# Performance work log

Measured on AMD Instinct MI355X. Metric: run time of the kernel, lower is better.

## Reference

```python
import jax, jax.numpy as jnp
import numpy as np

CODEBOOK_SIZE = 1024
EMB_DIM = 256
BETA = 0.25


def setup_inputs() -> dict:
    key = jax.random.key(0)
    k1, k2 = jax.random.split(key)
    z = jax.random.normal(k1, (8, EMB_DIM, 16, 16, 16), dtype=jnp.float32)
    # torch init: uniform(-1/K, 1/K)
    emb = jax.random.uniform(k2, (CODEBOOK_SIZE, EMB_DIM), dtype=jnp.float32,
                             minval=-1.0 / CODEBOOK_SIZE, maxval=1.0 / CODEBOOK_SIZE)
    return {"z": z, "emb": emb}


def reference(z, emb):
    b, c, h, w, dd = z.shape
    K = emb.shape[0]
    # (b c h w d) -> (b h w d, c)
    zf = jnp.transpose(z, (0, 2, 3, 4, 1)).reshape(-1, c)  # [N, C]
    d = ((zf ** 2).sum(axis=1, keepdims=True)
         + (emb ** 2).sum(axis=1)
         - 2.0 * zf @ emb.T)  # [N, K]
    mean_distance = jnp.mean(d)
    idx = jnp.argmin(d, axis=1)  # [N]
    # one-hot @ codebook == gather
    zq = jnp.take(emb, idx, axis=0)  # [N, C]
    zq = jnp.transpose(zq.reshape(b, h, w, dd, c), (0, 4, 1, 2, 3))  # [b,c,h,w,d]
    loss = (jnp.mean((jax.lax.stop_gradient(zq) - z) ** 2)
            + BETA * jnp.mean((zq - jax.lax.stop_gradient(z)) ** 2))
    # straight-through estimator
    zq_st = z + jax.lax.stop_gradient(zq - z)
    # perplexity from code usage histogram (== mean of one-hot encodings)
    counts = jnp.zeros((K,), dtype=z.dtype).at[idx].add(1.0)
    e_mean = counts / idx.shape[0]
    perplexity = jnp.exp(-jnp.sum(e_mean * jnp.log(e_mean + 1e-10)))
    return zq_st, loss, perplexity, idx, mean_distance
```

## Files before the change

### kernel.cpp

```cpp
#include <hip/hip_runtime.h>
#include <math.h>

#define C 256
#define K 1024
#define SS 4096
#define NB 8
#define NN 32768
#define ZQ_ELEMS 8388608
#define OUT_LOSS 8388608
#define OUT_PERP 8388609
#define OUT_IDX  8388610
#define OUT_MD   8421378

#define WS_SZ2   0
#define WS_SE2   1
#define WS_LOSS  2
#define WS_ZSUM  8
#define WS_ESUM  264
#define WS_CNT   520
#define WS_E2R   1544
#define WS_Z2N   2568
#define WS_FLG   35336
#define WS_EH    68608
#define WS_CAND  330752

#define TC_FACT 1.8e-6f
#define TF_FACT 1.6e-6f
#define CAP 4
#define CAP_BIG 24
#define OV 7

typedef __attribute__((ext_vector_type(8))) short short8;
typedef __attribute__((ext_vector_type(4))) float f32x4;
typedef unsigned short u16;

__device__ inline u16 f2bf(float x) {
  unsigned u = __float_as_uint(x);
  unsigned r = (u + 0x7fffu + ((u >> 16) & 1u)) >> 16;
  return (u16)r;
}
__device__ inline float bf2f(u16 h) { return __uint_as_float(((unsigned)h) << 16); }

__device__ __forceinline__ void gl_lds16(const u16* g, u16* l) {
  __builtin_amdgcn_global_load_lds(
      (const __attribute__((address_space(1))) unsigned int*)g,
      (__attribute__((address_space(3))) unsigned int*)l,
      16, 0, 0);
}

__device__ inline float np_sumsq_256(const float* __restrict__ a) {
  float tot = 0.f;
  #pragma unroll
  for (int h = 0; h < 2; ++h) {
    const float* p = a + 128 * h;
    float r[8];
    #pragma unroll
    for (int j = 0; j < 8; ++j) r[j] = __fmul_rn(p[j], p[j]);
    for (int i = 8; i < 128; i += 8) {
      #pragma unroll
      for (int j = 0; j < 8; ++j) {
        float v = p[i + j];
        r[j] = __fadd_rn(r[j], __fmul_rn(v, v));
      }
    }
    float s01 = __fadd_rn(r[0], r[1]);
    float s23 = __fadd_rn(r[2], r[3]);
    float s45 = __fadd_rn(r[4], r[5]);
    float s67 = __fadd_rn(r[6], r[7]);
    float res = __fadd_rn(__fadd_rn(s01, s23), __fadd_rn(s45, s67));
    tot = (h == 0) ? res : __fadd_rn(tot, res);
  }
  return tot;
}

__global__ __launch_bounds__(256)
void emb_prep_k(const float* __restrict__ emb, float* __restrict__ ws,
                u16* __restrict__ eh) {
  int r0 = blockIdx.x * 16;
  int t = threadIdx.x;
  float s = 0.f;
  #pragma unroll
  for (int i = 0; i < 16; ++i) {
    size_t idx = (size_t)(r0 + i) * C + t;
    float v = emb[idx];
    s += v;
    eh[idx] = f2bf(v);
  }
  atomicAdd(&ws[WS_ESUM + t], s);
  if (t < 16) {
    float e2 = np_sumsq_256(emb + (size_t)(r0 + t) * C);
    ws[WS_E2R + r0 + t] = e2;
    atomicAdd(&ws[WS_SE2], e2);
  }
}

#define MROWS 64
#define ZS_STRIDE 260

__global__ __launch_bounds__(256)
void prep_z_k(const float* __restrict__ z, float* __restrict__ ws,
              u16* __restrict__ zh_g) {
  __shared__ float zs[MROWS * ZS_STRIDE];
  const int t = threadIdx.x;
  const int n0 = blockIdx.x * MROWS;
  const int b = n0 / SS;
  const int s0 = n0 % SS;
  {
    const int sl = t & 63, cg = t >> 6;
    const float* zb = z + (size_t)b * C * SS + s0 + sl;
    #pragma unroll
    for (int i = 0; i < 16; ++i) {
      int c = (cg * 16 + i) * 4;
      float4 v;
      v.x = zb[(size_t)(c + 0) * SS];
      v.y = zb[(size_t)(c + 1) * SS];
      v.z = zb[(size_t)(c + 2) * SS];
      v.w = zb[(size_t)(c + 3) * SS];
      *(float4*)&zs[sl * ZS_STRIDE + c] = v;
    }
  }
  __syncthreads();
  {
    float s = 0.f;
    #pragma unroll 8
    for (int r = 0; r < MROWS; ++r) s += zs[r * ZS_STRIDE + t];
    atomicAdd(&ws[WS_ZSUM + t], s);
  }
  {
    #pragma unroll
    for (int i = 0; i < 8; ++i) {
      int q = i * 256 + t;
      int row = q >> 5;
      int c0 = (q & 31) * 8;
      float4 va = *(const float4*)&zs[row * ZS_STRIDE + c0];
      float4 vb = *(const float4*)&zs[row * ZS_STRIDE + c0 + 4];
      float f[8] = {va.x, va.y, va.z, va.w, vb.x, vb.y, vb.z, vb.w};
      short8 hv;
      #pragma unroll
      for (int j = 0; j < 8; ++j) hv[j] = (short)f2bf(f[j]);
      *(short8*)&zh_g[(size_t)(n0 + row) * C + c0] = hv;
    }
  }
  if (t < MROWS) {
    float z2 = np_sumsq_256(&zs[t * ZS_STRIDE]);
    ws[WS_Z2N + n0 + t] = z2;
    #pragma unroll
    for (int off = 32; off; off >>= 1) z2 += __shfl_down(z2, off);
    if (t == 0) atomicAdd(&ws[WS_SZ2], z2);
  }
}

#define BM 64
#define BN 128
#define CH 64

__global__ __launch_bounds__(256, 2)
void vq_mfma_k(const u16* __restrict__ zh_g, const u16* __restrict__ eh_g,
               const float* __restrict__ e2row, const float* __restrict__ z2np,
               float* __restrict__ out_idx,
               int* __restrict__ qarr, u16* __restrict__ cand) {
  extern __shared__ u16 smem_u16[];
  u16* Bh4 = smem_u16;
  float* e2all = (float*)(Bh4 + 4 * BN * CH);
  float* z2s  = e2all + K;
  float* lval = z2s + BM;
  unsigned* Mlds = (unsigned*)(lval + BM * CAP_BIG);
  unsigned* cntl = Mlds + BM;
  u16* lidx = (u16*)(cntl + BM);

  const int t = threadIdx.x;
  const int lane = t & 63;
  const int wid = t >> 6;
  const int wm = wid >> 1, wn = wid & 1;
  const int quad = lane >> 4, lr = lane & 15;
  const int row0 = blockIdx.x * BM;
  const int wrow = lane >> 3;
  const int pl = wrow * C + ((lane & 7) ^ wrow) * 8;

  #pragma unroll
  for (int i = 0; i < 4; ++i) e2all[i * 256 + t] = e2row[i * 256 + t];
  if (t < BM) {
    z2s[t] = z2np[row0 + t];
    Mlds[t] = 0x7F800000u;
    cntl[t] = 0u;
  }
  short8 areg[4][2][2];
  #pragma unroll
  for (int ch = 0; ch < 4; ++ch)
    #pragma unroll
    for (int s = 0; s < 2; ++s)
      #pragma unroll
      for (int mi = 0; mi < 2; ++mi)
        areg[ch][s][mi] = *(const short8*)
          &zh_g[(size_t)(row0 + wm * 32 + mi * 16 + lr) * C + ch * CH + (s * 4 + quad) * 8];

  auto stageB = [&](int j) {
    u16* Bb = Bh4 + (j & 3) * (BN * CH);
    const u16* srcb = eh_g + (size_t)(j >> 2) * (BN * C) + (j & 3) * CH;
    #pragma unroll
    for (int i = 0; i < 4; ++i) {
      int grow = (wid * 4 + i) * 8;
      gl_lds16(&srcb[(size_t)grow * C + pl], &Bb[grow * CH]);
    }
  };
  stageB(0);
  stageB(1);
  __syncthreads();

  float v1[8], i1f[8];
  #pragma unroll
  for (int s = 0; s < 8; ++s) { v1[s] = 3.4e38f; i1f[s] = 0.f; }
  f32x4 acc[2][4];
  #pragma unroll
  for (int mi = 0; mi < 2; ++mi)
    #pragma unroll
    for (int ni = 0; ni < 4; ++ni) acc[mi][ni] = (f32x4){0.f, 0.f, 0.f, 0.f};

  for (int nt = 0; nt < 8; ++nt) {
    #pragma unroll
    for (int ch = 0; ch < 4; ++ch) {
      const int it = nt * 4 + ch;
      if (ch < 2) stageB(it + 2);
      else if (nt < 7) stageB(it + 2);
      if (ch < 2) {
        asm volatile("s_waitcnt vmcnt(8) lgkmcnt(0)" ::: "memory");
      } else if (ch == 2) {
        if (nt < 7) asm volatile("s_waitcnt vmcnt(8) lgkmcnt(0)" ::: "memory");
        else        asm volatile("s_waitcnt vmcnt(4) lgkmcnt(0)" ::: "memory");
      } else {
        if (nt < 7) asm volatile("s_waitcnt vmcnt(8) lgkmcnt(0)" ::: "memory");
        else        asm volatile("s_waitcnt vmcnt(0) lgkmcnt(0)" ::: "memory");
      }
      __builtin_amdgcn_s_barrier();
      const u16* Bb = Bh4 + ch * (BN * CH);
      #pragma unroll
      for (int s = 0; s < 2; ++s) {
        #pragma unroll
        for (int ni = 0; ni < 4; ++ni) {
          int rowb = wn * 64 + ni * 16 + lr;
          int jp = (s * 4 + quad) ^ (rowb & 7);
          short8 bh = *(const short8*)&Bb[rowb * CH + jp * 8];
          #pragma unroll
          for (int mi = 0; mi < 2; ++mi)
            acc[mi][ni] = __builtin_amdgcn_mfma_f32_16x16x32_bf16(
                areg[ch][s][mi], bh, acc[mi][ni], 0, 0, 0);
        }
      }
      if (ch == 3) {
        const int kc0 = nt * BN;
        #pragma unroll
        for (int mi = 0; mi < 2; ++mi)
          #pragma unroll
          for (int r = 0; r < 4; ++r) {
            const int slot = mi * 4 + r;
            const int row = wm * 32 + mi * 16 + quad * 4 + r;
            const float z2r = z2s[row];
            float dqv[4];
            #pragma unroll
            for (int ni = 0; ni < 4; ++ni)
              dqv[ni] = __fsub_rn(__fadd_rn(z2r, e2all[kc0 + wn * 64 + ni * 16 + lr]),
                                  __fmul_rn(2.f, acc[mi][ni][r]));
            float mm = fminf(fminf(dqv[0], dqv[1]), fminf(dqv[2], dqv[3]));
            #pragma unroll
            for (int off = 1; off < 16; off <<= 1)
              mm = fminf(mm, __shfl_xor(mm, off));
            if (lr == 0) atomicMin(&Mlds[row], __float_as_uint(mm));
            float Mst = __uint_as_float(Mlds[row]);
            float base = fminf(mm, Mst);
            float thr = fmaf(base, TC_FACT, base);
            #pragma unroll
            for (int ni = 0; ni < 4; ++ni) {
              float dq = dqv[ni];
              int col = kc0 + wn * 64 + ni * 16 + lr;
              if (dq < v1[slot]) { v1[slot] = dq; i1f[slot] = (float)col; }
              if (dq < thr) {
                unsigned pp = atomicAdd(&cntl[row], 1u);
                if (pp < CAP_BIG) {
                  lval[row * CAP_BIG + pp] = dq;
                  lidx[row * CAP_BIG + pp] = (u16)col;
                }
              }
              acc[mi][ni][r] = 0.f;
            }
          }
      }
    }
  }

  #pragma unroll
  for (int off = 1; off < 16; off <<= 1) {
    #pragma unroll
    for (int s = 0; s < 8; ++s) {
      float ov1 = __shfl_xor(v1[s], off);
      float oi1 = __shfl_xor(i1f[s], off);
      bool take = (ov1 < v1[s]) || (ov1 == v1[s] && oi1 < i1f[s]);
      if (take) { v1[s] = ov1; i1f[s] = oi1; }
    }
  }
  __syncthreads();
  float* mv1 = (float*)Bh4;
  float* mi1 = mv1 + 2 * BM;
  if (lr == 0) {
    #pragma unroll
    for (int mi = 0; mi < 2; ++mi)
      #pragma unroll
      for (int r = 0; r < 4; ++r) {
        int slot = mi * 4 + r;
        int row = wm * 32 + mi * 16 + quad * 4 + r;
        mv1[wn * BM + row] = v1[slot];
        mi1[wn * BM + row] = i1f[slot];
      }
  }
  __syncthreads();
  if (t < BM) {
    float a1 = mv1[t], ai = mi1[t];
    float c1 = mv1[BM + t], ci = mi1[BM + t];
    bool take = (c1 < a1) || (c1 == a1 && ci < ai);
    float b1 = take ? c1 : a1;
    float bi = take ? ci : ai;
    out_idx[row0 + t] = bi;
    unsigned raw = cntl[t];
    float tf = fmaf(b1, TF_FACT, b1);
    int c = 0;
    u16 keep[CAP];
    bool ovf = raw > (unsigned)CAP_BIG;
    if (!ovf) {
      for (unsigned j = 0; j < raw; ++j) {
        if (lval[t * CAP_BIG + j] <= tf) {
          if (c < CAP) keep[c] = lidx[t * CAP_BIG + j];
          ++c;
        }
      }
      if (c > CAP) ovf = true;
    }
    if (ovf) {
      int o = atomicAdd(&qarr[1], 1);
      qarr[2 + NN - 1 - o] = row0 + t;
    } else if (c > 1) {
      int q = atomicAdd(&qarr[0], 1);
      qarr[2 + q] = (row0 + t) | (c << 16);
      #pragma unroll
      for (int j = 0; j < CAP; ++j)
        cand[(size_t)q * CAP + j] = (j < c) ? keep[j] : (u16)0;
    }
  }
}

__global__ __launch_bounds__(256)
void fixup_k(const float* __restrict__ z, const float* __restrict__ emb,
             const float* __restrict__ e2np, const float* __restrict__ z2np,
             const int* __restrict__ qarr, const u16* __restrict__ cand,
             float* __restrict__ out_idx) {
  int qcnt = qarr[0];
  if (qcnt > NN) qcnt = NN;
  const int t = threadIdx.x;
  const int lane = t & 63, w = t >> 6;
  for (int q = blockIdx.x * 4 + w; q < qcnt; q += gridDim.x * 4) {
    int e = qarr[2 + q];
    int n = e & 0xffff;
    int c = e >> 16;
    int b = n >> 12, s = n & (SS - 1);
    float z2 = z2np[n];
    const float* zb = z + (((size_t)b * C) << 12) + s;
    float4 zv;
    zv.x = zb[((size_t)(lane * 4 + 0)) << 12];
    zv.y = zb[((size_t)(lane * 4 + 1)) << 12];
    zv.z = zb[((size_t)(lane * 4 + 2)) << 12];
    zv.w = zb[((size_t)(lane * 4 + 3)) << 12];
    float bestd = 3.4e38f;
    int besti = 0x7fffffff;
    for (int j = 0; j < c; ++j) {
      int kk = (int)cand[(size_t)q * CAP + j];
      const float4 ev = *(const float4*)&emb[(size_t)kk * C + lane * 4];
      double acc = (double)zv.x * (double)ev.x;
      acc = fma((double)zv.y, (double)ev.y, acc);
      acc = fma((double)zv.z, (double)ev.z, acc);
      acc = fma((double)zv.w, (double)ev.w, acc);
      #pragma unroll
      for (int off = 32; off; off >>= 1) acc += __shfl_xor(acc, off);
      float g  = (float)acc;
      float t1 = __fadd_rn(z2, e2np[kk]);
      float d  = __fsub_rn(t1, __fmul_rn(2.f, g));
      if (d < bestd || (d == bestd && kk < besti)) { bestd = d; besti = kk; }
    }
    if (lane == 0) out_idx[n] = (float)besti;
  }
}

__global__ __launch_bounds__(256)
void fixov_k(const float* __restrict__ z, const float* __restrict__ emb,
             const float* __restrict__ e2np, const float* __restrict__ z2np,
             const int* __restrict__ qarr, float* __restrict__ out_idx) {
  __shared__ float zrow[C];
  __shared__ float bv[4];
  __shared__ int   bx[4];
  int novr = qarr[1];
  if (novr > NN) novr = NN;
  const int t = threadIdx.x;
  const int lane = t & 63, w = t >> 6;
  for (int o = blockIdx.x; o < novr; o += gridDim.x) {
    int n = qarr[2 + NN - 1 - o];
    int b = n >> 12, s = n & (SS - 1);
    __syncthreads();
    zrow[t] = z[((size_t)(b * C + t) << 12) + s];
    __syncthreads();
    float z2 = z2np[n];
    float best = 3.4e38f; int besti = 0x7fffffff;
    for (int kk = t; kk < K; kk += 256) {
      const float* er = emb + (size_t)kk * C;
      double a0 = 0.0, a1 = 0.0, a2 = 0.0, a3 = 0.0;
      for (int c = 0; c < C; c += 4) {
        a0 = fma((double)zrow[c + 0], (double)er[c + 0], a0);
        a1 = fma((double)zrow[c + 1], (double)er[c + 1], a1);
        a2 = fma((double)zrow[c + 2], (double)er[c + 2], a2);
        a3 = fma((double)zrow[c + 3], (double)er[c + 3], a3);
      }
      float g = (float)((a0 + a1) + (a2 + a3));
      float t1 = __fadd_rn(z2, e2np[kk]);
      float d  = __fsub_rn(t1, __fmul_rn(2.f, g));
      if (d < best || (d == best && kk < besti)) { best = d; besti = kk; }
    }
    #pragma unroll
    for (int off = 32; off; off >>= 1) {
      float ov = __shfl_down(best, off);
      int   oi = __shfl_down(besti, off);
      if (ov < best || (ov == best && oi < besti)) { best = ov; besti = oi; }
    }
    if (lane == 0) { bv[w] = best; bx[w] = besti; }
    __syncthreads();
    if (t == 0) {
      #pragma unroll
      for (int w2 = 1; w2 < 4; ++w2)
        if (bv[w2] < best || (bv[w2] == best && bx[w2] < besti)) {
          best = bv[w2]; besti = bx[w2];
        }
      out_idx[n] = (float)besti;
    }
  }
}

#define GROWS 64
__global__ __launch_bounds__(256)
void gather2_k(const float* __restrict__ z, const float* __restrict__ emb,
               float* __restrict__ out, float* __restrict__ ws,
               float* __restrict__ counts) {
  __shared__ float eb[GROWS * 257];
  __shared__ int idxs[GROWS];
  __shared__ float sc[4];
  const int t = threadIdx.x;
  const int n0 = blockIdx.x * GROWS;
  const int b = n0 >> 12;
  const int s0 = n0 & (SS - 1);
  if (t < GROWS) {
    int id = (int)out[OUT_IDX + n0 + t];
    idxs[t] = id;
    atomicAdd(&counts[id], 1.0f);
  }
  __syncthreads();
  #pragma unroll
  for (int i = 0; i < 16; ++i) {
    int q = i * 256 + t;
    int row = q >> 6, c4 = q & 63;
    float4 v = *(const float4*)&emb[(size_t)idxs[row] * C + c4 * 4];
    int base = row * 257 + c4 * 4;
    eb[base + 0] = v.x; eb[base + 1] = v.y;
    eb[base + 2] = v.z; eb[base + 3] = v.w;
  }
  __syncthreads();
  const int sl = t & 63, cg = t >> 6;
  const float* zb = z + (size_t)b * C * SS + s0 + sl;
  float* ob = out + (size_t)b * C * SS + s0 + sl;
  float l = 0.f;
  #pragma unroll 4
  for (int i = 0; i < 64; ++i) {
    int c = cg * 64 + i;
    float q = eb[sl * 257 + c];
    float zv = zb[(size_t)c * SS];
    float d = q - zv;
    l += d * d;
    ob[(size_t)c * SS] = q;
  }
  #pragma unroll
  for (int off = 32; off; off >>= 1) l += __shfl_down(l, off);
  int lane = t & 63, w = t >> 6;
  if (lane == 0) sc[w] = l;
  __syncthreads();
  if (t == 0)
    atomicAdd(&ws[WS_LOSS], sc[0] + sc[1] + sc[2] + sc[3]);
}

__global__ void finalize_k(const float* __restrict__ ws, float* __restrict__ out) {
  __shared__ float sc[8];
  int t = threadIdx.x;
  float ent = 0.f;
  #pragma unroll
  for (int k = t; k < K; k += 256) {
    float em = ws[WS_CNT + k] * (1.0f / NN);
    ent += em * logf(em + 1e-10f);
  }
  float zd = ws[WS_ZSUM + t] * ws[WS_ESUM + t];
  #pragma unroll
  for (int off = 32; off; off >>= 1) {
    ent += __shfl_down(ent, off);
    zd  += __shfl_down(zd, off);
  }
  int lane = t & 63, w = t >> 6;
  if (lane == 0) { sc[w] = ent; sc[4 + w] = zd; }
  __syncthreads();
  if (t == 0) {
    ent = sc[0] + sc[1] + sc[2] + sc[3];
    zd  = sc[4] + sc[5] + sc[6] + sc[7];
    out[OUT_LOSS] = 1.25f * ws[WS_LOSS] * (1.0f / ZQ_ELEMS);
    out[OUT_PERP] = expf(-ent);
    out[OUT_MD]   = ws[WS_SZ2] * (1.0f / NN) + ws[WS_SE2] * (1.0f / K)
                  - 2.0f * zd * (1.0f / ((float)NN * (float)K));
  }
}

extern "C" void kernel_launch(void* const* d_in, const int* in_sizes, int n_in,
                              void* d_out, int out_size, void* d_ws, size_t ws_size,
                              hipStream_t stream) {
  const float* z   = (const float*)d_in[0];
  const float* emb = (const float*)d_in[1];
  float* out = (float*)d_out;
  float* ws  = (float*)d_ws;
  int* qarr = (int*)(ws + WS_FLG);
  u16* cand = (u16*)(ws + WS_CAND);
  u16* eh_g = (u16*)(ws + WS_EH);
  u16* zh_g = (u16*)d_out;
  (void)in_sizes; (void)n_in; (void)out_size; (void)ws_size;

  hipMemsetAsync(d_ws, 0, WS_E2R * sizeof(float), stream);
  hipMemsetAsync(ws + WS_FLG, 0, 2 * sizeof(int), stream);
  emb_prep_k<<<64, 256, 0, stream>>>(emb, ws, eh_g);
  prep_z_k<<<NN / MROWS, 256, 0, stream>>>(z, ws, zh_g);
  size_t lds = (size_t)(4 * BN * CH) * sizeof(u16)
             + (size_t)(K + BM + BM * CAP_BIG) * sizeof(float)
             + (size_t)(2 * BM) * sizeof(unsigned)
             + (size_t)(BM * CAP_BIG) * sizeof(u16);
  vq_mfma_k<<<NN / BM, 256, lds, stream>>>(zh_g, eh_g,
                                           ws + WS_E2R, ws + WS_Z2N,
                                           out + OUT_IDX, qarr, cand);
  fixup_k<<<2048, 256, 0, stream>>>(z, emb, ws + WS_E2R, ws + WS_Z2N,
                                    qarr, cand, out + OUT_IDX);
  fixov_k<<<512, 256, 0, stream>>>(z, emb, ws + WS_E2R, ws + WS_Z2N,
                                   qarr, out + OUT_IDX);
  gather2_k<<<NN / GROWS, 256, 0, stream>>>(z, emb, out, ws, ws + WS_CNT);
  finalize_k<<<1, 256, 0, stream>>>(ws, out);
}
```

Baseline: 233.5 us.

## Split distance GEMM across eight waves and deepen the LDS prefetch pipeline

The fused distance/argmin kernel now runs 512 threads per block, with each wave owning 16 rows instead of 32. This halves the per-wave accumulator and argmin state and adds waves to hide latency. The codebook staging pipeline now prefetches three chunks ahead, issued after each barrier into the buffer just freed, with sched_barriers to pin the ordering and adjusted waitcnts. In exchange, each B fragment read from LDS feeds half as many MFMAs, so LDS traffic per FLOP rises, and the larger block may limit occupancy.

```diff
diff --git a/kernel.cpp b/kernel.cpp
--- a/kernel.cpp
+++ b/kernel.cpp
@@ -154,7 +154,7 @@
 #define BN 128
 #define CH 64
 
-__global__ __launch_bounds__(256, 2)
+__global__ __launch_bounds__(512, 2)
 void vq_mfma_k(const u16* __restrict__ zh_g, const u16* __restrict__ eh_g,
                const float* __restrict__ e2row, const float* __restrict__ z2np,
                float* __restrict__ out_idx,
@@ -171,67 +171,66 @@
   const int t = threadIdx.x;
   const int lane = t & 63;
   const int wid = t >> 6;
-  const int wm = wid >> 1, wn = wid & 1;
+  const int wm = wid >> 1;
+  const int wn = wid & 1;
   const int quad = lane >> 4, lr = lane & 15;
   const int row0 = blockIdx.x * BM;
   const int wrow = lane >> 3;
   const int pl = wrow * C + ((lane & 7) ^ wrow) * 8;
 
   #pragma unroll
-  for (int i = 0; i < 4; ++i) e2all[i * 256 + t] = e2row[i * 256 + t];
+  for (int i = 0; i < 2; ++i) e2all[i * 512 + t] = e2row[i * 512 + t];
   if (t < BM) {
     z2s[t] = z2np[row0 + t];
     Mlds[t] = 0x7F800000u;
     cntl[t] = 0u;
   }
-  short8 areg[4][2][2];
+  short8 areg[4][2];
   #pragma unroll
   for (int ch = 0; ch < 4; ++ch)
     #pragma unroll
     for (int s = 0; s < 2; ++s)
-      #pragma unroll
-      for (int mi = 0; mi < 2; ++mi)
-        areg[ch][s][mi] = *(const short8*)
-          &zh_g[(size_t)(row0 + wm * 32 + mi * 16 + lr) * C + ch * CH + (s * 4 + quad) * 8];
+      areg[ch][s] = *(const short8*)
+        &zh_g[(size_t)(row0 + wm * 16 + lr) * C + ch * CH + (s * 4 + quad) * 8];
 
   auto stageB = [&](int j) {
     u16* Bb = Bh4 + (j & 3) * (BN * CH);
     const u16* srcb = eh_g + (size_t)(j >> 2) * (BN * C) + (j & 3) * CH;
     #pragma unroll
-    for (int i = 0; i < 4; ++i) {
-      int grow = (wid * 4 + i) * 8;
+    for (int i = 0; i < 2; ++i) {
+      int grow = (wid * 2 + i) * 8;
       gl_lds16(&srcb[(size_t)grow * C + pl], &Bb[grow * CH]);
     }
   };
   stageB(0);
   stageB(1);
-  __syncthreads();
-
-  float v1[8], i1f[8];
-  #pragma unroll
-  for (int s = 0; s < 8; ++s) { v1[s] = 3.4e38f; i1f[s] = 0.f; }
-  f32x4 acc[2][4];
-  #pragma unroll
-  for (int mi = 0; mi < 2; ++mi)
-    #pragma unroll
-    for (int ni = 0; ni < 4; ++ni) acc[mi][ni] = (f32x4){0.f, 0.f, 0.f, 0.f};
+  stageB(2);
+
+  float v1[4], i1f[4];
+  #pragma unroll
+  for (int s = 0; s < 4; ++s) { v1[s] = 3.4e38f; i1f[s] = 0.f; }
+  f32x4 acc[4];
+  #pragma unroll
+  for (int ni = 0; ni < 4; ++ni) acc[ni] = (f32x4){0.f, 0.f, 0.f, 0.f};
 
   for (int nt = 0; nt < 8; ++nt) {
     #pragma unroll
     for (int ch = 0; ch < 4; ++ch) {
       const int it = nt * 4 + ch;
-      if (ch < 2) stageB(it + 2);
-      else if (nt < 7) stageB(it + 2);
+      __builtin_amdgcn_sched_barrier(0);
       if (ch < 2) {
-        asm volatile("s_waitcnt vmcnt(8) lgkmcnt(0)" ::: "memory");
+        asm volatile("s_waitcnt vmcnt(4) lgkmcnt(0)" ::: "memory");
       } else if (ch == 2) {
-        if (nt < 7) asm volatile("s_waitcnt vmcnt(8) lgkmcnt(0)" ::: "memory");
-        else        asm volatile("s_waitcnt vmcnt(4) lgkmcnt(0)" ::: "memory");
+        if (nt < 7) asm volatile("s_waitcnt vmcnt(4) lgkmcnt(0)" ::: "memory");
+        else        asm volatile("s_waitcnt vmcnt(2) lgkmcnt(0)" ::: "memory");
       } else {
-        if (nt < 7) asm volatile("s_waitcnt vmcnt(8) lgkmcnt(0)" ::: "memory");
+        if (nt < 7) asm volatile("s_waitcnt vmcnt(4) lgkmcnt(0)" ::: "memory");
         else        asm volatile("s_waitcnt vmcnt(0) lgkmcnt(0)" ::: "memory");
       }
       __builtin_amdgcn_s_barrier();
+      __builtin_amdgcn_sched_barrier(0);
+      if (nt < 7) stageB(it + 3);
+      else if (ch == 0) stageB(31);
       const u16* Bb = Bh4 + ch * (BN * CH);
       #pragma unroll
       for (int s = 0; s < 2; ++s) {
@@ -240,49 +239,44 @@
           int rowb = wn * 64 + ni * 16 + lr;
           int jp = (s * 4 + quad) ^ (rowb & 7);
           short8 bh = *(const short8*)&Bb[rowb * CH + jp * 8];
-          #pragma unroll
-          for (int mi = 0; mi < 2; ++mi)
-            acc[mi][ni] = __builtin_amdgcn_mfma_f32_16x16x32_bf16(
-                areg[ch][s][mi], bh, acc[mi][ni], 0, 0, 0);
+          acc[ni] = __builtin_amdgcn_mfma_f32_16x16x32_bf16(
+              areg[ch][s], bh, acc[ni], 0, 0, 0);
         }
       }
       if (ch == 3) {
         const int kc0 = nt * BN;
         #pragma unroll
-        for (int mi = 0; mi < 2; ++mi)
+        for (int r = 0; r < 4; ++r) {
+          const int row = wm * 16 + quad * 4 + r;
+          const float z2r = z2s[row];
+          float dqv[4];
           #pragma unroll
-          for (int r = 0; r < 4; ++r) {
-            const int slot = mi * 4 + r;
-            const int row = wm * 32 + mi * 16 + quad * 4 + r;
-            const float z2r = z2s[row];
-            float dqv[4];
-            #pragma unroll
-            for (int ni = 0; ni < 4; ++ni)
-              dqv[ni] = __fsub_rn(__fadd_rn(z2r, e2all[kc0 + wn * 64 + ni * 16 + lr]),
-                                  __fmul_rn(2.f, acc[mi][ni][r]));
-            float mm = fminf(fminf(dqv[0], dqv[1]), fminf(dqv[2], dqv[3]));
-            #pragma unroll
-            for (int off = 1; off < 16; off <<= 1)
-              mm = fminf(mm, __shfl_xor(mm, off));
-            if (lr == 0) atomicMin(&Mlds[row], __float_as_uint(mm));
-            float Mst = __uint_as_float(Mlds[row]);
-            float base = fminf(mm, Mst);
-            float thr = fmaf(base, TC_FACT, base);
-            #pragma unroll
-            for (int ni = 0; ni < 4; ++ni) {
-              float dq = dqv[ni];
-              int col = kc0 + wn * 64 + ni * 16 + lr;
-              if (dq < v1[slot]) { v1[slot] = dq; i1f[slot] = (float)col; }
-              if (dq < thr) {
-                unsigned pp = atomicAdd(&cntl[row], 1u);
-                if (pp < CAP_BIG) {
-                  lval[row * CAP_BIG + pp] = dq;
-                  lidx[row * CAP_BIG + pp] = (u16)col;
-                }
+          for (int ni = 0; ni < 4; ++ni)
+            dqv[ni] = __fsub_rn(__fadd_rn(z2r, e2all[kc0 + wn * 64 + ni * 16 + lr]),
+                                __fmul_rn(2.f, acc[ni][r]));
+          float mm = fminf(fminf(dqv[0], dqv[1]), fminf(dqv[2], dqv[3]));
+          #pragma unroll
+          for (int off = 1; off < 16; off <<= 1)
+            mm = fminf(mm, __shfl_xor(mm, off));
+          if (lr == 0) atomicMin(&Mlds[row], __float_as_uint(mm));
+          float Mst = __uint_as_float(Mlds[row]);
+          float base = fminf(mm, Mst);
+          float thr = fmaf(base, TC_FACT, base);
+          #pragma unroll
+          for (int ni = 0; ni < 4; ++ni) {
+            float dq = dqv[ni];
+            int col = kc0 + wn * 64 + ni * 16 + lr;
+            if (dq < v1[r]) { v1[r] = dq; i1f[r] = (float)col; }
+            if (dq < thr) {
+              unsigned pp = atomicAdd(&cntl[row], 1u);
+              if (pp < CAP_BIG) {
+                lval[row * CAP_BIG + pp] = dq;
+                lidx[row * CAP_BIG + pp] = (u16)col;
               }
-              acc[mi][ni][r] = 0.f;
             }
+            acc[ni][r] = 0.f;
           }
+        }
       }
     }
   }
@@ -290,7 +284,7 @@
   #pragma unroll
   for (int off = 1; off < 16; off <<= 1) {
     #pragma unroll
-    for (int s = 0; s < 8; ++s) {
+    for (int s = 0; s < 4; ++s) {
       float ov1 = __shfl_xor(v1[s], off);
       float oi1 = __shfl_xor(i1f[s], off);
       bool take = (ov1 < v1[s]) || (ov1 == v1[s] && oi1 < i1f[s]);
@@ -302,14 +296,11 @@
   float* mi1 = mv1 + 2 * BM;
   if (lr == 0) {
     #pragma unroll
-    for (int mi = 0; mi < 2; ++mi)
-      #pragma unroll
-      for (int r = 0; r < 4; ++r) {
-        int slot = mi * 4 + r;
-        int row = wm * 32 + mi * 16 + quad * 4 + r;
-        mv1[wn * BM + row] = v1[slot];
-        mi1[wn * BM + row] = i1f[slot];
-      }
+    for (int r = 0; r < 4; ++r) {
+      int row = wm * 16 + quad * 4 + r;
+      mv1[wn * BM + row] = v1[r];
+      mi1[wn * BM + row] = i1f[r];
+    }
   }
   __syncthreads();
   if (t < BM) {
@@ -538,7 +529,7 @@
              + (size_t)(K + BM + BM * CAP_BIG) * sizeof(float)
              + (size_t)(2 * BM) * sizeof(unsigned)
              + (size_t)(BM * CAP_BIG) * sizeof(u16);
-  vq_mfma_k<<<NN / BM, 256, lds, stream>>>(zh_g, eh_g,
+  vq_mfma_k<<<NN / BM, 512, lds, stream>>>(zh_g, eh_g,
                                            ws + WS_E2R, ws + WS_Z2N,
                                            out + OUT_IDX, qarr, cand);
   fixup_k<<<2048, 256, 0, stream>>>(z, emb, ws + WS_E2R, ws + WS_Z2N,
```

Result: faster. 222.0 us (-4.9%).
